# Performance work log

Measured on AMD Instinct MI355X. Metric: run time of the kernel, lower is better.

## Reference

```python
import jax, jax.numpy as jnp
import numpy as np

NUM_GROUPS = 64  # matches fill_max of ids; all groups present w.h.p. so unique-inverse == ids


def setup_inputs() -> dict:
    key = jax.random.key(0)
    ks = jax.random.split(key, 8)
    B, N, D = 8, 8192, 512
    s = 1.0 / np.sqrt(D)
    return {
        "x": jax.random.normal(ks[0], (B, N, D), dtype=jnp.float32),
        "ids": jax.random.randint(ks[1], (N,), 0, NUM_GROUPS),
        "w1": jax.random.normal(ks[2], (D, D), dtype=jnp.float32) * s,
        "b1": jax.random.normal(ks[3], (D,), dtype=jnp.float32) * s,
        "w2": jax.random.normal(ks[4], (D, D), dtype=jnp.float32) * s,
        "b2": jax.random.normal(ks[5], (D,), dtype=jnp.float32) * s,
        "w3": jax.random.normal(ks[6], (D, D), dtype=jnp.float32) * s,
        "b3": jax.random.normal(ks[7], (D,), dtype=jnp.float32) * s,
    }


def reference(x, ids, w1, b1, w2, b2, w3, b3):
    # x: [B, N, D]; ids: [N] group labels in [0, NUM_GROUPS)
    G = NUM_GROUPS
    a = jnp.einsum('bnd,ed->bne', x, w1) + b1          # linear1 logits
    v = jnp.einsum('bnd,ed->bne', x, w2) + b2          # linear2 values
    # move segment axis to front: [N, B, D]
    aT = jnp.transpose(a, (1, 0, 2))
    vT = jnp.transpose(v, (1, 0, 2))
    # per-group stable softmax along the segment axis
    mx = jax.lax.stop_gradient(jax.ops.segment_max(aT, ids, num_segments=G))  # [G,B,D]
    ex = jnp.exp(aT - mx[ids])
    denom = jax.ops.segment_sum(ex, ids, num_segments=G)                      # [G,B,D]
    wts = ex / denom[ids]                                                     # [N,B,D]
    # weighted scatter-sum of values -> [G, B, D] -> [B, G, D]
    y = jnp.transpose(jax.ops.segment_sum(vT * wts, ids, num_segments=G), (1, 0, 2))
    out = jnp.einsum('bgd,ed->bge', y, w3) + b3        # linear3
    # expand: gather group outputs back to per-element rows -> [B, N, D]
    return out[:, ids]
```

## Files before the change

kernel.cpp:

```cpp
#include <hip/hip_runtime.h>
#include <hip/hip_bf16.h>
#include <math.h>

#define B_ 8
#define N_ 8192
#define D_ 512
#define G_ 64
#define M_ (B_ * N_)
#define NF 1024
#define SPLIT 8
#define LSTRIDE 256

typedef short bf16x8 __attribute__((ext_vector_type(8)));
typedef float f32x4 __attribute__((ext_vector_type(4)));

__device__ __forceinline__ unsigned short f2bf(float f) {
    __hip_bfloat16 h = __float2bfloat16(f);
    return *reinterpret_cast<unsigned short*>(&h);
}
__device__ __forceinline__ float bf2f(unsigned int bits16) {
    return __uint_as_float(bits16 << 16);
}
__device__ __forceinline__ void gload_lds16(const void* g, void* l) {
    __builtin_amdgcn_global_load_lds((const __attribute__((address_space(1))) void*)g,
                                     (__attribute__((address_space(3))) void*)l,
                                     16, 0, 0);
}

__global__ __launch_bounds__(256) void cast_x(const float* __restrict__ x,
                                              unsigned short* __restrict__ xb) {
    size_t t = (size_t)blockIdx.x * 256 + threadIdx.x;
    float4 f = *(const float4*)(x + t * 4);
    ushort4 u;
    u.x = f2bf(f.x); u.y = f2bf(f.y); u.z = f2bf(f.z); u.w = f2bf(f.w);
    *(ushort4*)(xb + t * 4) = u;
}

__global__ __launch_bounds__(256) void cast_w(const float* __restrict__ w1,
                                              const float* __restrict__ b1,
                                              const float* __restrict__ w2,
                                              const float* __restrict__ b2,
                                              unsigned short* __restrict__ wB,
                                              float* __restrict__ biasB) {
    int t = blockIdx.x * 256 + threadIdx.x;
    int idx = t * 4;
    int row = idx >> 9;
    int col = idx & 511;
    const float* src = (row < 512) ? (w1 + (size_t)row * 512 + col)
                                   : (w2 + (size_t)(row - 512) * 512 + col);
    float4 f = *(const float4*)src;
    ushort4 u;
    u.x = f2bf(f.x); u.y = f2bf(f.y); u.z = f2bf(f.z); u.w = f2bf(f.w);
    *(ushort4*)(wB + idx) = u;
    if (t < 1024) biasB[t] = (t < 512) ? b1[t] : b2[t - 512];
}

__global__ __launch_bounds__(256) void build_lists2(const int* __restrict__ ids,
                                                    int* __restrict__ counts,
                                                    int* __restrict__ list) {
    __shared__ int sid[N_];
    __shared__ int scnt[256];
    const int g = blockIdx.x;
    const int t = threadIdx.x;
    for (int i = t; i < N_; i += 256) sid[i] = ids[i];
    __syncthreads();
    int c = 0;
    const int nb = t * 32;
#pragma unroll 8
    for (int k = 0; k < 32; ++k) c += (sid[nb + k] == g) ? 1 : 0;
    scnt[t] = c;
    __syncthreads();
    if (t == 0) {
        int run = 0;
        for (int i = 0; i < 256; ++i) { int x = scnt[i]; scnt[i] = run; run += x; }
        counts[g] = run;
    }
    __syncthreads();
    int pos = g * LSTRIDE + scnt[t];
    for (int k = 0; k < 32; ++k)
        if (sid[nb + k] == g) list[pos++] = nb + k;
}

__global__ __launch_bounds__(256) void gemm12_mfma(const unsigned short* __restrict__ xb,
                                                   const unsigned short* __restrict__ wB,
                                                   const float* __restrict__ biasB,
                                                   unsigned short* __restrict__ av) {
    __shared__ unsigned short ls[2][2][128 * 64];

    const int o    = blockIdx.x;
    const int rX   = o & 7;
    const int slot = o >> 3;
    const int n_t  = slot & 7;
    const int m_t  = (slot >> 3) * 8 + rX;
    const int m0 = m_t * 128;
    const int n0 = n_t * 128;

    const int tid = threadIdx.x;
    const int l = tid & 63;
    const int w = tid >> 6;
    const int wm = w >> 1, wn = w & 1;

    const int lr = l >> 3;
    const int lc = (l & 7) * 8;

    const int fr = l & 15;
    const int ko = (l >> 4) * 8;
    const int r4 = (l >> 4) * 4;

    f32x4 acc[4][4];
#pragma unroll
    for (int i = 0; i < 4; ++i)
#pragma unroll
        for (int j = 0; j < 4; ++j) acc[i][j] = (f32x4){0.f, 0.f, 0.f, 0.f};

    auto stageT = [&](int buf, int kt) {
#pragma unroll
        for (int q = 0; q < 4; ++q) {
            const int c = w * 4 + q;
            const int row = c * 8 + lr;
            gload_lds16(xb + (size_t)(m0 + row) * 512 + kt + lc, &ls[buf][0][c * 512]);
            gload_lds16(wB + (size_t)(n0 + row) * 512 + kt + lc, &ls[buf][1][c * 512]);
        }
    };

    stageT(0, 0);
    __syncthreads();
    int cur = 0;
    for (int t = 0; t < 8; ++t) {
        if (t < 7) stageT(cur ^ 1, (t + 1) * 64);
#pragma unroll
        for (int ks = 0; ks < 2; ++ks) {
            bf16x8 af[4], bfr[4];
#pragma unroll
            for (int i = 0; i < 4; ++i)
                af[i] = *(const bf16x8*)&ls[cur][0][(wm * 64 + i * 16 + fr) * 64 + ks * 32 + ko];
#pragma unroll
            for (int j = 0; j < 4; ++j)
                bfr[j] = *(const bf16x8*)&ls[cur][1][(wn * 64 + j * 16 + fr) * 64 + ks * 32 + ko];
#pragma unroll
            for (int i = 0; i < 4; ++i)
#pragma unroll
                for (int j = 0; j < 4; ++j)
                    acc[i][j] = __builtin_amdgcn_mfma_f32_16x16x32_bf16(af[i], bfr[j], acc[i][j], 0, 0, 0);
        }
        __syncthreads();
        cur ^= 1;
    }

    unsigned short* tf = &ls[0][0][0];
#pragma unroll
    for (int j = 0; j < 4; ++j) {
        const int lcol = wn * 64 + j * 16 + fr;
        const float bj = biasB[n0 + lcol];
#pragma unroll
        for (int i = 0; i < 4; ++i) {
            const int lrow0 = wm * 64 + i * 16 + r4;
#pragma unroll
            for (int rr2 = 0; rr2 < 4; ++rr2) {
                const int row = lrow0 + rr2;
                const int byteOff = row * 256 + ((lcol * 2) ^ (((row >> 2) & 7) << 5));
                tf[byteOff >> 1] = f2bf(acc[i][j][rr2] + bj);
            }
        }
    }
    __syncthreads();
#pragma unroll
    for (int p = 0; p < 8; ++p) {
        const int row = p * 16 + (tid >> 4);
        const int cc = (tid & 15) * 8;
        const int byteOff = row * 256 + ((cc * 2) ^ (((row >> 2) & 7) << 5));
        uint4 val = *(const uint4*)((const char*)tf + byteOff);
        *(uint4*)(av + (size_t)(m0 + row) * NF + n0 + cc) = val;
    }
}

__global__ __launch_bounds__(256) void softaggA(const unsigned short* __restrict__ av,
                                                const int* __restrict__ counts,
                                                const int* __restrict__ list,
                                                float* __restrict__ pd,
                                                float* __restrict__ py) {
    const int g = blockIdx.x, b = blockIdx.y, s = blockIdx.z;
    const int e0 = threadIdx.x * 2;
    const int cnt = counts[g];
    float d0 = 0.f, d1 = 0.f, y0 = 0.f, y1 = 0.f;
    for (int i = s; i < cnt; i += SPLIT) {
        const int n = list[g * LSTRIDE + i];
        const unsigned short* row = av + (size_t)(b * N_ + n) * NF;
        const unsigned pa = *(const unsigned*)(row + e0);
        const unsigned pv = *(const unsigned*)(row + 512 + e0);
        const float a0 = bf2f(pa & 0xFFFFu);
        const float a1 = __uint_as_float(pa & 0xFFFF0000u);
        const float v0 = bf2f(pv & 0xFFFFu);
        const float v1 = __uint_as_float(pv & 0xFFFF0000u);
        const float ea0 = __expf(a0), ea1 = __expf(a1);
        d0 += ea0; d1 += ea1;
        y0 = fmaf(ea0, v0, y0); y1 = fmaf(ea1, v1, y1);
    }
    const size_t o = (((size_t)s * G_ + g) * B_ + b) * D_ + e0;
    pd[o] = d0; pd[o + 1] = d1;
    py[o] = y0; py[o + 1] = y1;
}

__global__ __launch_bounds__(256) void combineB(const float* __restrict__ pd,
                                                const float* __restrict__ py,
                                                float* __restrict__ y) {
    const int g = blockIdx.x, b = blockIdx.y;
    const int e0 = threadIdx.x * 2;
    float d0 = 0.f, d1 = 0.f, s0 = 0.f, s1 = 0.f;
#pragma unroll
    for (int s = 0; s < SPLIT; ++s) {
        const size_t o = (((size_t)s * G_ + g) * B_ + b) * D_ + e0;
        d0 += pd[o]; d1 += pd[o + 1];
        s0 += py[o]; s1 += py[o + 1];
    }
    const size_t yo = ((size_t)b * G_ + g) * D_ + e0;
    y[yo] = s0 / d0;
    y[yo + 1] = s1 / d1;
}

__global__ __launch_bounds__(256) void gemm3(const float* __restrict__ y,
                                             const float* __restrict__ w3,
                                             const float* __restrict__ b3,
                                             float* __restrict__ out_small) {
    __shared__ float ys[16][68];
    __shared__ float wss[16][68];
    const int m0 = blockIdx.x * 64;
    const int n0 = blockIdx.y * 64;
    const int tid = threadIdx.x;
    const int tr = tid >> 4;
    const int tc = tid & 15;
    const int lrow = tid >> 2;
    const int lk4 = (tid & 3) * 4;

    float acc[4][4] = {};

    for (int k0 = 0; k0 < D_; k0 += 16) {
        float4 yv = *(const float4*)(y + (size_t)(m0 + lrow) * D_ + k0 + lk4);
        float4 wv = *(const float4*)(w3 + (size_t)(n0 + lrow) * D_ + k0 + lk4);
        __syncthreads();
        ys[lk4 + 0][lrow] = yv.x;  ys[lk4 + 1][lrow] = yv.y;
        ys[lk4 + 2][lrow] = yv.z;  ys[lk4 + 3][lrow] = yv.w;
        wss[lk4 + 0][lrow] = wv.x; wss[lk4 + 1][lrow] = wv.y;
        wss[lk4 + 2][lrow] = wv.z; wss[lk4 + 3][lrow] = wv.w;
        __syncthreads();
#pragma unroll
        for (int kk = 0; kk < 16; ++kk) {
            float4 y4 = *(const float4*)&ys[kk][tr * 4];
            float4 w4 = *(const float4*)&wss[kk][tc * 4];
            float ya[4] = {y4.x, y4.y, y4.z, y4.w};
            float wa[4] = {w4.x, w4.y, w4.z, w4.w};
#pragma unroll
            for (int i = 0; i < 4; ++i)
#pragma unroll
                for (int j = 0; j < 4; ++j)
                    acc[i][j] = fmaf(ya[i], wa[j], acc[i][j]);
        }
    }

    float bb[4];
#pragma unroll
    for (int j = 0; j < 4; ++j) bb[j] = b3[n0 + tc * 4 + j];
#pragma unroll
    for (int i = 0; i < 4; ++i) {
        size_t o = (size_t)(m0 + tr * 4 + i) * D_ + n0 + tc * 4;
        float4 r;
        r.x = acc[i][0] + bb[0]; r.y = acc[i][1] + bb[1];
        r.z = acc[i][2] + bb[2]; r.w = acc[i][3] + bb[3];
        *(float4*)(out_small + o) = r;
    }
}

__global__ __launch_bounds__(256) void gather_out(const int* __restrict__ ids,
                                                  const float* __restrict__ out_small,
                                                  float* __restrict__ out) {
    const int c = blockIdx.x * 256 + threadIdx.x;
    const int per_row = D_ / 4;
    const int b = c / (N_ * per_row);
    const int rem = c % (N_ * per_row);
    const int n = rem / per_row;
    const int q = rem % per_row;
    const int g = ids[n];
    float4 val = *(const float4*)(out_small + ((size_t)b * G_ + g) * D_ + q * 4);
    *(float4*)(out + (size_t)c * 4) = val;
}

extern "C" void kernel_launch(void* const* d_in, const int* in_sizes, int n_in,
                              void* d_out, int out_size, void* d_ws, size_t ws_size,
                              hipStream_t stream) {
    (void)in_sizes; (void)n_in; (void)out_size; (void)ws_size;
    const float* x   = (const float*)d_in[0];
    const int*   ids = (const int*)d_in[1];
    const float* w1  = (const float*)d_in[2];
    const float* b1  = (const float*)d_in[3];
    const float* w2  = (const float*)d_in[4];
    const float* b2  = (const float*)d_in[5];
    const float* w3  = (const float*)d_in[6];
    const float* b3  = (const float*)d_in[7];
    float* out = (float*)d_out;

    unsigned short* av = (unsigned short*)d_out;

    float* ws_f = (float*)d_ws;
    unsigned short* xb = (unsigned short*)ws_f;
    float* after_xb  = ws_f + 16777216;
    unsigned short* wB = (unsigned short*)after_xb;
    float* biasB     = after_xb + 262144;
    float* pd        = biasB + 1024;
    float* py        = pd + 2097152;
    float* y         = py + 2097152;
    float* out_small = y + 262144;
    int*   list      = (int*)(out_small + 262144);
    int*   counts    = list + G_ * LSTRIDE;

    hipLaunchKernelGGL(cast_x, dim3(32768), dim3(256), 0, stream, x, xb);
    hipLaunchKernelGGL(cast_w, dim3(512), dim3(256), 0, stream, w1, b1, w2, b2, wB, biasB);
    hipLaunchKernelGGL(build_lists2, dim3(G_), dim3(256), 0, stream, ids, counts, list);
    hipLaunchKernelGGL(gemm12_mfma, dim3(4096), dim3(256), 0, stream, xb, wB, biasB, av);
    hipLaunchKernelGGL(softaggA, dim3(G_, B_, SPLIT), dim3(256), 0, stream,
                       av, counts, list, pd, py);
    hipLaunchKernelGGL(combineB, dim3(G_, B_), dim3(256), 0, stream, pd, py, y);
    hipLaunchKernelGGL(gemm3, dim3(8, 8), dim3(256), 0, stream, y, w3, b3, out_small);
    hipLaunchKernelGGL(gather_out, dim3(32768), dim3(256), 0, stream, ids, out_small, out);
}
```

Before: 225.3 us.

## Fuse segment softmax-aggregation into GEMM epilogue using group-sorted row permutation

Builds a group-sorted permutation of rows in a single block, then has the GEMM gather x rows in that order so each 128-row tile spans at most four groups. The epilogue computes exp(a) and exp(a)*v and reduces them per group inside the tile, writing small partials instead of the full bf16 a/v intermediate. A new combine kernel sums the partials across tiles. This removes the large intermediate write and the gather-based reread in softaggA, but it assumes at most four groups per tile and drops max-subtraction. It also adds LDS XOR swizzling to the staging.

```diff
diff --git a/kernel.cpp b/kernel.cpp
--- a/kernel.cpp
+++ b/kernel.cpp
@@ -7,9 +7,6 @@
 #define D_ 512
 #define G_ 64
 #define M_ (B_ * N_)
-#define NF 1024
-#define SPLIT 8
-#define LSTRIDE 256
 
 typedef short bf16x8 __attribute__((ext_vector_type(8)));
 typedef float f32x4 __attribute__((ext_vector_type(4)));
@@ -17,9 +14,6 @@
 __device__ __forceinline__ unsigned short f2bf(float f) {
     __hip_bfloat16 h = __float2bfloat16(f);
     return *reinterpret_cast<unsigned short*>(&h);
-}
-__device__ __forceinline__ float bf2f(unsigned int bits16) {
-    return __uint_as_float(bits16 << 16);
 }
 __device__ __forceinline__ void gload_lds16(const void* g, void* l) {
     __builtin_amdgcn_global_load_lds((const __attribute__((address_space(1))) void*)g,
@@ -55,71 +49,106 @@
     if (t < 1024) biasB[t] = (t < 512) ? b1[t] : b2[t - 512];
 }
 
-__global__ __launch_bounds__(256) void build_lists2(const int* __restrict__ ids,
+__global__ __launch_bounds__(256) void build_lists3(const int* __restrict__ ids,
                                                     int* __restrict__ counts,
-                                                    int* __restrict__ list) {
+                                                    int* __restrict__ baseO,
+                                                    int* __restrict__ fgO,
+                                                    int* __restrict__ perm) {
     __shared__ int sid[N_];
-    __shared__ int scnt[256];
-    const int g = blockIdx.x;
+    __shared__ unsigned short hist[256][G_];
+    __shared__ int sbase[G_ + 1];
     const int t = threadIdx.x;
     for (int i = t; i < N_; i += 256) sid[i] = ids[i];
-    __syncthreads();
-    int c = 0;
+#pragma unroll
+    for (int g = 0; g < G_; ++g) hist[t][g] = 0;
+    __syncthreads();
     const int nb = t * 32;
-#pragma unroll 8
-    for (int k = 0; k < 32; ++k) c += (sid[nb + k] == g) ? 1 : 0;
-    scnt[t] = c;
+    for (int k = 0; k < 32; ++k) hist[t][sid[nb + k]]++;
+    __syncthreads();
+    if (t < G_) {
+        int run = 0;
+        for (int i = 0; i < 256; ++i) {
+            int v = hist[i][t];
+            hist[i][t] = (unsigned short)run;
+            run += v;
+        }
+        counts[t] = run;
+    }
     __syncthreads();
     if (t == 0) {
-        int run = 0;
-        for (int i = 0; i < 256; ++i) { int x = scnt[i]; scnt[i] = run; run += x; }
-        counts[g] = run;
-    }
-    __syncthreads();
-    int pos = g * LSTRIDE + scnt[t];
-    for (int k = 0; k < 32; ++k)
-        if (sid[nb + k] == g) list[pos++] = nb + k;
-}
-
-__global__ __launch_bounds__(256) void gemm12_mfma(const unsigned short* __restrict__ xb,
-                                                   const unsigned short* __restrict__ wB,
-                                                   const float* __restrict__ biasB,
-                                                   unsigned short* __restrict__ av) {
-    __shared__ unsigned short ls[2][2][128 * 64];
-
-    const int o    = blockIdx.x;
-    const int rX   = o & 7;
-    const int slot = o >> 3;
-    const int n_t  = slot & 7;
-    const int m_t  = (slot >> 3) * 8 + rX;
-    const int m0 = m_t * 128;
-    const int n0 = n_t * 128;
+        int acc = 0;
+        for (int g = 0; g < G_; ++g) { sbase[g] = acc; acc += counts[g]; }
+        sbase[G_] = acc;
+    }
+    __syncthreads();
+    if (t < G_) baseO[t] = sbase[t];
+    if (t < G_) {
+        const int row = t * 128;
+        int g = 0;
+        while (g + 1 < G_ && sbase[g + 1] <= row) ++g;
+        fgO[t] = g;
+    }
+    for (int k = 0; k < 32; ++k) {
+        const int n = nb + k;
+        const int g = sid[n];
+        const int pos = sbase[g] + hist[t][g];
+        hist[t][g]++;
+        perm[pos] = n;
+    }
+}
+
+__global__ __launch_bounds__(256) void gemm_fused(const unsigned short* __restrict__ xb,
+                                                  const unsigned short* __restrict__ wB,
+                                                  const float* __restrict__ biasB,
+                                                  const int* __restrict__ perm,
+                                                  const int* __restrict__ base,
+                                                  const int* __restrict__ fg,
+                                                  float* __restrict__ pt) {
+    __shared__ unsigned short lsA[2][128 * 64];
+    __shared__ unsigned short lsB[2][2][64 * 64];
+
+    const int o  = blockIdx.x;
+    const int mt = (o & 7) + ((o >> 6) << 3);
+    const int et = (o >> 3) & 7;
+    const int b  = mt >> 6;
+    const int tl = mt & 63;
+    const int r0 = tl * 128;
 
     const int tid = threadIdx.x;
     const int l = tid & 63;
     const int w = tid >> 6;
     const int wm = w >> 1, wn = w & 1;
-
     const int lr = l >> 3;
-    const int lc = (l & 7) * 8;
-
+    const int lslot = l & 7;
     const int fr = l & 15;
-    const int ko = (l >> 4) * 8;
-    const int r4 = (l >> 4) * 4;
-
-    f32x4 acc[4][4];
+    const int scol = 8 * (lslot ^ lr);
+
+    int nrow[4];
+#pragma unroll
+    for (int q = 0; q < 4; ++q) nrow[q] = perm[r0 + (w * 4 + q) * 8 + lr];
+
+    f32x4 acc_a[4][2], acc_v[4][2];
 #pragma unroll
     for (int i = 0; i < 4; ++i)
 #pragma unroll
-        for (int j = 0; j < 4; ++j) acc[i][j] = (f32x4){0.f, 0.f, 0.f, 0.f};
+        for (int j = 0; j < 2; ++j) {
+            acc_a[i][j] = (f32x4){0.f, 0.f, 0.f, 0.f};
+            acc_v[i][j] = (f32x4){0.f, 0.f, 0.f, 0.f};
+        }
 
     auto stageT = [&](int buf, int kt) {
 #pragma unroll
         for (int q = 0; q < 4; ++q) {
             const int c = w * 4 + q;
-            const int row = c * 8 + lr;
-            gload_lds16(xb + (size_t)(m0 + row) * 512 + kt + lc, &ls[buf][0][c * 512]);
-            gload_lds16(wB + (size_t)(n0 + row) * 512 + kt + lc, &ls[buf][1][c * 512]);
+            gload_lds16(xb + (((size_t)(b << 13) + nrow[q]) << 9) + kt + scol,
+                        &lsA[buf][c * 512]);
+        }
+#pragma unroll
+        for (int q = 0; q < 4; ++q) {
+            const int p = q >> 1;
+            const int c2 = (w << 1) | (q & 1);
+            const int wr = p * 512 + et * 64 + c2 * 8 + lr;
+            gload_lds16(wB + ((size_t)wr << 9) + kt + scol, &lsB[buf][p][c2 * 512]);
         }
     };
 
@@ -130,92 +159,113 @@
         if (t < 7) stageT(cur ^ 1, (t + 1) * 64);
 #pragma unroll
         for (int ks = 0; ks < 2; ++ks) {
-            bf16x8 af[4], bfr[4];
+            const int ib = 8 * ((ks * 4 + (l >> 4)) ^ (fr & 7));
+            bf16x8 af[4], bq[2][2];
 #pragma unroll
             for (int i = 0; i < 4; ++i)
-                af[i] = *(const bf16x8*)&ls[cur][0][(wm * 64 + i * 16 + fr) * 64 + ks * 32 + ko];
-#pragma unroll
-            for (int j = 0; j < 4; ++j)
-                bfr[j] = *(const bf16x8*)&ls[cur][1][(wn * 64 + j * 16 + fr) * 64 + ks * 32 + ko];
+                af[i] = *(const bf16x8*)&lsA[cur][(wm * 64 + i * 16 + fr) * 64 + ib];
+#pragma unroll
+            for (int p = 0; p < 2; ++p)
+#pragma unroll
+                for (int j = 0; j < 2; ++j)
+                    bq[p][j] = *(const bf16x8*)&lsB[cur][p][(wn * 32 + j * 16 + fr) * 64 + ib];
 #pragma unroll
             for (int i = 0; i < 4; ++i)
 #pragma unroll
-                for (int j = 0; j < 4; ++j)
-                    acc[i][j] = __builtin_amdgcn_mfma_f32_16x16x32_bf16(af[i], bfr[j], acc[i][j], 0, 0, 0);
+                for (int j = 0; j < 2; ++j) {
+                    acc_a[i][j] = __builtin_amdgcn_mfma_f32_16x16x32_bf16(af[i], bq[0][j], acc_a[i][j], 0, 0, 0);
+                    acc_v[i][j] = __builtin_amdgcn_mfma_f32_16x16x32_bf16(af[i], bq[1][j], acc_v[i][j], 0, 0, 0);
+                }
         }
         __syncthreads();
         cur ^= 1;
     }
 
-    unsigned short* tf = &ls[0][0][0];
-#pragma unroll
-    for (int j = 0; j < 4; ++j) {
-        const int lcol = wn * 64 + j * 16 + fr;
-        const float bj = biasB[n0 + lcol];
-#pragma unroll
-        for (int i = 0; i < 4; ++i) {
-            const int lrow0 = wm * 64 + i * 16 + r4;
-#pragma unroll
-            for (int rr2 = 0; rr2 < 4; ++rr2) {
-                const int row = lrow0 + rr2;
-                const int byteOff = row * 256 + ((lcol * 2) ^ (((row >> 2) & 7) << 5));
-                tf[byteOff >> 1] = f2bf(acc[i][j][rr2] + bj);
+    const int fg0 = fg[tl];
+    const int bnd0 = (fg0 + 1 < G_) ? base[fg0 + 1] : (1 << 30);
+    const int bnd1 = (fg0 + 2 < G_) ? base[fg0 + 2] : (1 << 30);
+    const int bnd2 = (fg0 + 3 < G_) ? base[fg0 + 3] : (1 << 30);
+    float b1c[2], b2c[2];
+#pragma unroll
+    for (int j = 0; j < 2; ++j) {
+        const int col = et * 64 + wn * 32 + j * 16 + fr;
+        b1c[j] = biasB[col];
+        b2c[j] = biasB[512 + col];
+    }
+    float dpart[4][2] = {}, ypart[4][2] = {};
+    const int rbase = r0 + wm * 64 + ((l >> 4) << 2);
+#pragma unroll
+    for (int i = 0; i < 4; ++i)
+#pragma unroll
+        for (int rr = 0; rr < 4; ++rr) {
+            const int row = rbase + i * 16 + rr;
+            const int s = (row >= bnd0) + (row >= bnd1) + (row >= bnd2);
+#pragma unroll
+            for (int j = 0; j < 2; ++j) {
+                const float e = __expf(acc_a[i][j][rr] + b1c[j]);
+                const float ey = e * (acc_v[i][j][rr] + b2c[j]);
+#pragma unroll
+                for (int s2 = 0; s2 < 4; ++s2) {
+                    dpart[s2][j] += (s == s2) ? e : 0.f;
+                    ypart[s2][j] += (s == s2) ? ey : 0.f;
+                }
             }
         }
-    }
-    __syncthreads();
-#pragma unroll
-    for (int p = 0; p < 8; ++p) {
-        const int row = p * 16 + (tid >> 4);
-        const int cc = (tid & 15) * 8;
-        const int byteOff = row * 256 + ((cc * 2) ^ (((row >> 2) & 7) << 5));
-        uint4 val = *(const uint4*)((const char*)tf + byteOff);
-        *(uint4*)(av + (size_t)(m0 + row) * NF + n0 + cc) = val;
-    }
-}
-
-__global__ __launch_bounds__(256) void softaggA(const unsigned short* __restrict__ av,
+#pragma unroll
+    for (int s2 = 0; s2 < 4; ++s2)
+#pragma unroll
+        for (int j = 0; j < 2; ++j) {
+            dpart[s2][j] += __shfl_xor(dpart[s2][j], 16);
+            dpart[s2][j] += __shfl_xor(dpart[s2][j], 32);
+            ypart[s2][j] += __shfl_xor(ypart[s2][j], 16);
+            ypart[s2][j] += __shfl_xor(ypart[s2][j], 32);
+        }
+    float* red = (float*)&lsA[0][0];
+    if ((l >> 4) == 0) {
+#pragma unroll
+        for (int s2 = 0; s2 < 4; ++s2)
+#pragma unroll
+            for (int j = 0; j < 2; ++j) {
+                const int colL = wn * 32 + j * 16 + fr;
+                red[((wm * 4 + s2) * 64 + colL) * 2 + 0] = dpart[s2][j];
+                red[((wm * 4 + s2) * 64 + colL) * 2 + 1] = ypart[s2][j];
+            }
+    }
+    __syncthreads();
+#pragma unroll
+    for (int k = 0; k < 2; ++k) {
+        const int idx = tid * 2 + k;
+        const int dy = idx & 1;
+        const int colL = (idx >> 1) & 63;
+        const int s2 = idx >> 7;
+        const float vsum = red[((0 * 4 + s2) * 64 + colL) * 2 + dy] +
+                           red[((1 * 4 + s2) * 64 + colL) * 2 + dy];
+        pt[((((size_t)(b * 64 + tl)) * 4 + s2) * 512 + et * 64 + colL) * 2 + dy] = vsum;
+    }
+}
+
+__global__ __launch_bounds__(256) void combineC(const float* __restrict__ pt,
+                                                const int* __restrict__ base,
                                                 const int* __restrict__ counts,
-                                                const int* __restrict__ list,
-                                                float* __restrict__ pd,
-                                                float* __restrict__ py) {
-    const int g = blockIdx.x, b = blockIdx.y, s = blockIdx.z;
-    const int e0 = threadIdx.x * 2;
-    const int cnt = counts[g];
-    float d0 = 0.f, d1 = 0.f, y0 = 0.f, y1 = 0.f;
-    for (int i = s; i < cnt; i += SPLIT) {
-        const int n = list[g * LSTRIDE + i];
-        const unsigned short* row = av + (size_t)(b * N_ + n) * NF;
-        const unsigned pa = *(const unsigned*)(row + e0);
-        const unsigned pv = *(const unsigned*)(row + 512 + e0);
-        const float a0 = bf2f(pa & 0xFFFFu);
-        const float a1 = __uint_as_float(pa & 0xFFFF0000u);
-        const float v0 = bf2f(pv & 0xFFFFu);
-        const float v1 = __uint_as_float(pv & 0xFFFF0000u);
-        const float ea0 = __expf(a0), ea1 = __expf(a1);
-        d0 += ea0; d1 += ea1;
-        y0 = fmaf(ea0, v0, y0); y1 = fmaf(ea1, v1, y1);
-    }
-    const size_t o = (((size_t)s * G_ + g) * B_ + b) * D_ + e0;
-    pd[o] = d0; pd[o + 1] = d1;
-    py[o] = y0; py[o + 1] = y1;
-}
-
-__global__ __launch_bounds__(256) void combineB(const float* __restrict__ pd,
-                                                const float* __restrict__ py,
+                                                const int* __restrict__ fg,
                                                 float* __restrict__ y) {
     const int g = blockIdx.x, b = blockIdx.y;
-    const int e0 = threadIdx.x * 2;
-    float d0 = 0.f, d1 = 0.f, s0 = 0.f, s1 = 0.f;
-#pragma unroll
-    for (int s = 0; s < SPLIT; ++s) {
-        const size_t o = (((size_t)s * G_ + g) * B_ + b) * D_ + e0;
-        d0 += pd[o]; d1 += pd[o + 1];
-        s0 += py[o]; s1 += py[o + 1];
-    }
-    const size_t yo = ((size_t)b * G_ + g) * D_ + e0;
-    y[yo] = s0 / d0;
-    y[yo + 1] = s1 / d1;
+    const int bs = base[g];
+    int cnt = counts[g];
+    if (cnt == 0) cnt = 1;
+    const int t0 = bs >> 7, t1 = (bs + cnt - 1) >> 7;
+    for (int c = threadIdx.x; c < 512; c += 256) {
+        float d = 0.f, yy = 0.f;
+        for (int t = t0; t <= t1; ++t) {
+            const int s = g - fg[t];
+            if (s >= 0 && s < 4) {
+                const float* p = &pt[((((size_t)(b * 64 + t)) * 4 + s) * 512 + c) * 2];
+                d += p[0];
+                yy += p[1];
+            }
+        }
+        y[((size_t)(b * G_ + g)) * 512 + c] = yy / d;
+    }
 }
 
 __global__ __launch_bounds__(256) void gemm3(const float* __restrict__ y,
@@ -298,27 +348,25 @@
     const float* b3  = (const float*)d_in[7];
     float* out = (float*)d_out;
 
-    unsigned short* av = (unsigned short*)d_out;
-
     float* ws_f = (float*)d_ws;
     unsigned short* xb = (unsigned short*)ws_f;
     float* after_xb  = ws_f + 16777216;
     unsigned short* wB = (unsigned short*)after_xb;
     float* biasB     = after_xb + 262144;
-    float* pd        = biasB + 1024;
-    float* py        = pd + 2097152;
-    float* y         = py + 2097152;
+    float* pt        = biasB + 1024;
+    float* y         = pt + 2097152;
     float* out_small = y + 262144;
-    int*   list      = (int*)(out_small + 262144);
-    int*   counts    = list + G_ * LSTRIDE;
+    int*   perm      = (int*)(out_small + 262144);
+    int*   base      = perm + N_;
+    int*   counts    = base + G_;
+    int*   fg        = counts + G_;
 
     hipLaunchKernelGGL(cast_x, dim3(32768), dim3(256), 0, stream, x, xb);
     hipLaunchKernelGGL(cast_w, dim3(512), dim3(256), 0, stream, w1, b1, w2, b2, wB, biasB);
-    hipLaunchKernelGGL(build_lists2, dim3(G_), dim3(256), 0, stream, ids, counts, list);
-    hipLaunchKernelGGL(gemm12_mfma, dim3(4096), dim3(256), 0, stream, xb, wB, biasB, av);
-    hipLaunchKernelGGL(softaggA, dim3(G_, B_, SPLIT), dim3(256), 0, stream,
-                       av, counts, list, pd, py);
-    hipLaunchKernelGGL(combineB, dim3(G_, B_), dim3(256), 0, stream, pd, py, y);
+    hipLaunchKernelGGL(build_lists3, dim3(1), dim3(256), 0, stream, ids, counts, base, fg, perm);
+    hipLaunchKernelGGL(gemm_fused, dim3(4096), dim3(256), 0, stream,
+                       xb, wB, biasB, perm, base, fg, pt);
+    hipLaunchKernelGGL(combineC, dim3(G_, B_), dim3(256), 0, stream, pt, base, counts, fg, y);
     hipLaunchKernelGGL(gemm3, dim3(8, 8), dim3(256), 0, stream, y, w3, b3, out_small);
     hipLaunchKernelGGL(gather_out, dim3(32768), dim3(256), 0, stream, ids, out_small, out);
 }
```

Measured after the change: 216.4 us. 4.0% less time.
